# Kernel optimization log

Hardware: AMD Instinct MI355X
Metric: run time of the kernel (lower is better)

The kernel has to match this reference:

```python
import jax, jax.numpy as jnp
import numpy as np

NUM_HEADS = 2
POOL_K = 256
REPEAT = 20


def setup_inputs() -> dict:
    key = jax.random.key(0)
    k1, k2, k3 = jax.random.split(key, 3)
    C = 6144
    d = C // NUM_HEADS                      # 3072
    N = REPEAT * (d // POOL_K)              # 240, required by Pq add
    x = jax.random.normal(k1, (N, C), dtype=jnp.float32)
    w_qkv = jax.random.normal(k2, (3 * C, C), dtype=jnp.float32) * 0.02
    w_proj = jax.random.normal(k3, (C, C), dtype=jnp.float32) * 0.02
    b_proj = jnp.zeros((C,), dtype=jnp.float32)
    return {"x": x, "w_qkv": w_qkv, "w_proj": w_proj, "b_proj": b_proj}


def reference(x, w_qkv, w_proj, b_proj):
    N, C = x.shape
    H = NUM_HEADS
    d = C // H
    scale = d ** -0.5
    # qkv: (N, 3C) -> (N, 3, H, d) -> (3, H, N, d)
    qkv = (x @ w_qkv.T).reshape(N, 3, H, d).transpose(1, 2, 0, 3)
    q, k, v = qkv[0], qkv[1], qkv[2]        # each (H, N, d)
    # MaxPool1d(256) over last dim, then tile x20 along last dim -> (H, N, N)
    Pq = q.reshape(H, N, d // POOL_K, POOL_K).max(axis=-1)
    Pq = jnp.tile(Pq, (1, 1, REPEAT))       # (H, N, N)
    attn = jnp.einsum('hnd,hmd->hnm', q, k) * scale + 0.1 * Pq
    attn = jax.nn.softmax(attn, axis=-1)
    out = jnp.einsum('hnm,hmd->hnd', attn, v)    # (H, N, d)
    out = out.transpose(1, 0, 2).reshape(N, C)
    return out @ w_proj.T + b_proj
```

## Files before the change

### kernel.cpp

```cpp
#include <hip/hip_runtime.h>
#include <hip/hip_bf16.h>

#define NN 240
#define CC 6144
#define DD 3072
#define C3 18432
#define HH 2

typedef __attribute__((ext_vector_type(8))) short bf16x8;
typedef __attribute__((ext_vector_type(4))) float f32x4;
typedef unsigned short ushort_t;

static __device__ __forceinline__ unsigned short f2bf(float f) {
    __hip_bfloat16 h = __float2bfloat16(f);
    return __builtin_bit_cast(unsigned short, h);
}

#define GLDS16(g, l) __builtin_amdgcn_global_load_lds( \
    (const __attribute__((address_space(1))) void*)(g), \
    (__attribute__((address_space(3))) void*)(l), 16, 0, 0)

__global__ __launch_bounds__(512, 4)
void gemm_bt4(const ushort_t* __restrict__ Ab, int lda, long long sAz,
              const float* __restrict__ B, int ldb, long long sBz,
              const float* __restrict__ bias,
              float* __restrict__ C0, long long sC0z,
              float* __restrict__ CP, long long sCPz,
              int ldc, int N, int Kc, int KS,
              ushort_t* __restrict__ Qb) {
    __shared__ ushort_t sA[2][256 * 64];
    __shared__ ushort_t sB[2][64 * 64];

    const int zc = blockIdx.z;
    const int z = zc / KS, kc = zc % KS;
    const ushort_t* Abase = Ab + (size_t)z * sAz + (size_t)kc * Kc;
    const float*    Bbase = B  + (size_t)z * sBz + (size_t)kc * Kc;
    float* Cw = (kc == 0) ? (C0 + (size_t)z * sC0z)
                          : (CP + (size_t)(z * (KS - 1) + kc - 1) * sCPz);

    const int n0 = blockIdx.x * 64;
    const int tid = threadIdx.x, lane = tid & 63, wid = tid >> 6;
    const int wm = wid >> 1, wn = wid & 1;
    const int l16 = lane & 15, lk = lane >> 4;

    const int arow = wid * 32 + (lane >> 3);
    const ushort_t* ap = Abase + (size_t)arow * lda
                         + ((lane & 7) ^ ((lane >> 3) & 7)) * 8;

    const int brow = tid >> 3, boct = tid & 7;
    const float* bp = Bbase + (size_t)(n0 + brow) * ldb + boct * 8;
    const int bws = brow * 64 + ((boct ^ (brow & 7)) * 8);

    f32x4 acc[4][2] = {};
    const int nt = Kc / 64;

    {
#pragma unroll
        for (int i = 0; i < 4; ++i)
            GLDS16(ap + (size_t)i * 8 * lda, &sA[0][(wid * 4 + i) * 512]);
        float4 f0 = *(const float4*)bp;
        float4 f1 = *(const float4*)(bp + 4);
        asm volatile("s_waitcnt vmcnt(0)" ::: "memory");
        bf16x8 r;
        r[0] = (short)f2bf(f0.x); r[1] = (short)f2bf(f0.y);
        r[2] = (short)f2bf(f0.z); r[3] = (short)f2bf(f0.w);
        r[4] = (short)f2bf(f1.x); r[5] = (short)f2bf(f1.y);
        r[6] = (short)f2bf(f1.z); r[7] = (short)f2bf(f1.w);
        *(bf16x8*)&sB[0][bws] = r;
        __syncthreads();
    }

    for (int t = 0; t < nt; ++t) {
        const int cur = t & 1, nxt = cur ^ 1;
        const bool pf = (t + 1 < nt);
        float4 f0, f1;
        if (pf) {
            const ushort_t* a = ap + (size_t)(t + 1) * 64;
#pragma unroll
            for (int i = 0; i < 4; ++i)
                GLDS16(a + (size_t)i * 8 * lda, &sA[nxt][(wid * 4 + i) * 512]);
            const float* p = bp + (size_t)(t + 1) * 64;
            f0 = *(const float4*)p;
            f1 = *(const float4*)(p + 4);
        }
        __builtin_amdgcn_sched_barrier(0);

        const char* As = (const char*)sA[cur];
        const char* Bs = (const char*)sB[cur];
#pragma unroll
        for (int ks = 0; ks < 2; ++ks) {
            bf16x8 af[4], bf[2];
#pragma unroll
            for (int mt = 0; mt < 4; ++mt) {
                int row = wm * 64 + mt * 16 + l16;
                int boff = row * 128 + (((ks * 4 + lk) * 16) ^ ((row & 7) << 4));
                af[mt] = *(const bf16x8*)(As + boff);
            }
#pragma unroll
            for (int nf = 0; nf < 2; ++nf) {
                int row = wn * 32 + nf * 16 + l16;
                int boff = row * 128 + (((ks * 4 + lk) * 16) ^ ((row & 7) << 4));
                bf[nf] = *(const bf16x8*)(Bs + boff);
            }
            __builtin_amdgcn_s_setprio(1);
#pragma unroll
            for (int mt = 0; mt < 4; ++mt)
#pragma unroll
                for (int nf = 0; nf < 2; ++nf)
                    acc[mt][nf] = __builtin_amdgcn_mfma_f32_16x16x32_bf16(
                        af[mt], bf[nf], acc[mt][nf], 0, 0, 0);
            __builtin_amdgcn_s_setprio(0);
        }
        __builtin_amdgcn_sched_barrier(0);

        if (pf) {
            asm volatile("s_waitcnt vmcnt(0)" ::: "memory");
            bf16x8 r;
            r[0] = (short)f2bf(f0.x); r[1] = (short)f2bf(f0.y);
            r[2] = (short)f2bf(f0.z); r[3] = (short)f2bf(f0.w);
            r[4] = (short)f2bf(f1.x); r[5] = (short)f2bf(f1.y);
            r[6] = (short)f2bf(f1.z); r[7] = (short)f2bf(f1.w);
            *(bf16x8*)&sB[nxt][bws] = r;
        }
        __syncthreads();
    }

#pragma unroll
    for (int mt = 0; mt < 4; ++mt) {
#pragma unroll
        for (int j = 0; j < 4; ++j) {
            int grow = wm * 64 + mt * 16 + lk * 4 + j;
            if (grow < NN) {
#pragma unroll
                for (int nf = 0; nf < 2; ++nf) {
                    int gcol = n0 + wn * 32 + nf * 16 + l16;
                    if (gcol < N) {
                        float v = acc[mt][nf][j];
                        if (kc == 0 && bias) v += bias[gcol];
                        Cw[(size_t)grow * ldc + gcol] = v;
                        if (Qb && gcol < CC)
                            Qb[(size_t)grow * CC + gcol] = f2bf(v);
                    }
                }
            }
        }
    }
}

__global__ __launch_bounds__(256)
void convert_kernel(const float* __restrict__ x, ushort_t* __restrict__ xb) {
    int id = blockIdx.x * 256 + threadIdx.x;
    int row = id / 768, c8 = id % 768;
    bf16x8 o = {};
    if (row < NN) {
        const float* p = x + (size_t)row * CC + c8 * 8;
        float4 a = *(const float4*)p, b = *(const float4*)(p + 4);
        o[0] = (short)f2bf(a.x); o[1] = (short)f2bf(a.y);
        o[2] = (short)f2bf(a.z); o[3] = (short)f2bf(a.w);
        o[4] = (short)f2bf(b.x); o[5] = (short)f2bf(b.y);
        o[6] = (short)f2bf(b.z); o[7] = (short)f2bf(b.w);
    }
    *(bf16x8*)(xb + (size_t)row * CC + c8 * 8) = o;
}

__global__ __launch_bounds__(256)
void reduce_proj(float4* __restrict__ o4, const float4* __restrict__ p4,
                 long long s4) {
    int i = blockIdx.x * 256 + threadIdx.x;
    float4 a = o4[i];
#pragma unroll
    for (int k = 0; k < 2; ++k) {
        float4 b = p4[(size_t)k * s4 + i];
        a.x += b.x; a.y += b.y; a.z += b.z; a.w += b.w;
    }
    o4[i] = a;
}

__global__ __launch_bounds__(256)
void qmax_kernel(const float* __restrict__ qkv, float* __restrict__ qmax) {
    int idx = blockIdx.x * 4 + (threadIdx.x >> 6);
    int lane = threadIdx.x & 63;
    int c = idx % 12;
    int r = idx / 12;
    int n = r % NN, h = r / NN;
    const float* p = qkv + (size_t)n * C3 + h * DD + c * 256 + lane * 4;
    float4 f = *(const float4*)p;
    float m = fmaxf(fmaxf(f.x, f.y), fmaxf(f.z, f.w));
#pragma unroll
    for (int off = 32; off >= 1; off >>= 1)
        m = fmaxf(m, __shfl_xor(m, off));
    if (lane == 0) qmax[idx] = m;
}

__global__ __launch_bounds__(256)
void softmax_kernel(float* __restrict__ attn, const float* __restrict__ gpart,
                    int ksm1, const float* __restrict__ qmax) {
    int r = blockIdx.x * 4 + (threadIdx.x >> 6);
    int lane = threadIdx.x & 63;
    int z = r / NN, n = r % NN;
    float* row = attn + (size_t)r * NN;
    const float* qm = qmax + r * 12;
    const float scale = 0.0180421959f;
    float v[4];
    float mx = -1e30f;
#pragma unroll
    for (int i = 0; i < 4; ++i) {
        int m = lane + 64 * i;
        v[i] = -1e30f;
        if (m < NN) {
            float s = row[m];
            for (int kc = 0; kc < ksm1; ++kc)
                s += gpart[(size_t)(z * ksm1 + kc) * (NN * NN)
                           + (size_t)n * NN + m];
            v[i] = s * scale + 0.1f * qm[m % 12];
        }
        mx = fmaxf(mx, v[i]);
    }
#pragma unroll
    for (int off = 32; off >= 1; off >>= 1)
        mx = fmaxf(mx, __shfl_xor(mx, off));
    float s = 0.f;
#pragma unroll
    for (int i = 0; i < 4; ++i) {
        v[i] = __expf(v[i] - mx);
        s += v[i];
    }
#pragma unroll
    for (int off = 32; off >= 1; off >>= 1)
        s += __shfl_xor(s, off);
    float inv = 1.0f / s;
#pragma unroll
    for (int i = 0; i < 4; ++i) {
        int m = lane + 64 * i;
        if (m < NN) row[m] = v[i] * inv;
    }
}

__global__ __launch_bounds__(256)
void pv_kernel(const float* __restrict__ attn, const float* __restrict__ qkv,
               ushort_t* __restrict__ preb) {
    const int h = blockIdx.z;
    const int n0 = blockIdx.y * 16;
    const int dd0 = blockIdx.x * 256;
    __shared__ float s_attn[16 * NN];
    for (int i = threadIdx.x; i < 16 * NN; i += 256)
        s_attn[i] = attn[(size_t)h * NN * NN + (n0 + i / NN) * NN + (i % NN)];
    __syncthreads();

    const float* vp = qkv + 2 * CC + h * DD + dd0 + threadIdx.x;
    float acc[16] = {};
    for (int m = 0; m < NN; m += 4) {
        float v0 = vp[(size_t)(m + 0) * C3];
        float v1 = vp[(size_t)(m + 1) * C3];
        float v2 = vp[(size_t)(m + 2) * C3];
        float v3 = vp[(size_t)(m + 3) * C3];
#pragma unroll
        for (int i = 0; i < 16; ++i) {
            float4 a = *(const float4*)&s_attn[i * NN + m];
            acc[i] += a.x * v0 + a.y * v1 + a.z * v2 + a.w * v3;
        }
    }
#pragma unroll
    for (int i = 0; i < 16; ++i)
        preb[(size_t)(n0 + i) * CC + h * DD + dd0 + threadIdx.x] =
            f2bf(acc[i]);
}

extern "C" void kernel_launch(void* const* d_in, const int* in_sizes, int n_in,
                              void* d_out, int out_size, void* d_ws, size_t ws_size,
                              hipStream_t stream) {
    const float* x      = (const float*)d_in[0];
    const float* w_qkv  = (const float*)d_in[1];
    const float* w_proj = (const float*)d_in[2];
    const float* b_proj = (const float*)d_in[3];
    float* out = (float*)d_out;

    const size_t f_qkv  = (size_t)NN * C3;
    const size_t f_attn = (size_t)HH * NN * NN;
    const size_t f_qmax = (size_t)HH * NN * 12;
    float* qkv   = (float*)d_ws;
    float* attn  = qkv + f_qkv;
    float* qmaxb = attn + f_attn;
    ushort_t* xb   = (ushort_t*)(qmaxb + f_qmax);
    ushort_t* qb   = xb + (size_t)256 * CC;
    ushort_t* preb = qb + (size_t)256 * CC;
    float* gpart = (float*)(preb + (size_t)256 * CC);

    convert_kernel<<<768, 256, 0, stream>>>(x, xb);

    gemm_bt4<<<dim3(C3 / 64, 1, 1), 512, 0, stream>>>(
        xb, CC, 0LL, w_qkv, CC, 0LL, nullptr,
        qkv, 0LL, gpart, 0LL,
        C3, C3, CC, 1, qb);

    qmax_kernel<<<1440, 256, 0, stream>>>(qkv, qmaxb);

    gemm_bt4<<<dim3(4, 1, HH * 16), 512, 0, stream>>>(
        qb, CC, (long long)DD,
        qkv + CC, C3, (long long)DD, nullptr,
        attn, (long long)(NN * NN), gpart, (long long)(NN * NN),
        NN, NN, DD / 16, 16, nullptr);

    softmax_kernel<<<120, 256, 0, stream>>>(attn, gpart, 15, qmaxb);

    pv_kernel<<<dim3(12, 15, HH), 256, 0, stream>>>(attn, qkv, preb);

    gemm_bt4<<<dim3(CC / 64, 1, 3), 512, 0, stream>>>(
        preb, CC, 0LL, w_proj, CC, 0LL, b_proj,
        out, 0LL, gpart, (long long)((size_t)NN * CC),
        CC, CC, CC / 3, 3, nullptr);
    reduce_proj<<<1440, 256, 0, stream>>>((float4*)out, (const float4*)gpart,
        (long long)((size_t)NN * CC / 4));
}
```

Baseline: 354.2 us.

## Deepen GEMM B-operand prefetch to two stages and raise QK split-K to 24

Restructures the bf16 MFMA GEMM main loop so the fp32 B tile is loaded two iterations ahead into alternating register sets. Waits use partial vmcnt counts instead of draining all outstanding loads, and the loop is unrolled by two so the register buffers swap roles. The aim is to hide global-load latency of the fp32 weight stream, which dominates these memory-bound GEMMs. Separately, the QK^T GEMM split-K grows from 16 to 24 chunks for more parallelism, with the softmax summing 23 partials. The unroll-by-two loop assumes an even tile count, and extra registers may lower occupancy.

```diff
diff --git a/kernel.cpp b/kernel.cpp
--- a/kernel.cpp
+++ b/kernel.cpp
@@ -21,13 +21,13 @@
     (__attribute__((address_space(3))) void*)(l), 16, 0, 0)
 
 __global__ __launch_bounds__(512, 4)
-void gemm_bt4(const ushort_t* __restrict__ Ab, int lda, long long sAz,
-              const float* __restrict__ B, int ldb, long long sBz,
-              const float* __restrict__ bias,
-              float* __restrict__ C0, long long sC0z,
-              float* __restrict__ CP, long long sCPz,
-              int ldc, int N, int Kc, int KS,
-              ushort_t* __restrict__ Qb) {
+void gemm_p2(const ushort_t* __restrict__ Ab, int lda, long long sAz,
+             const float* __restrict__ B, int ldb, long long sBz,
+             const float* __restrict__ bias,
+             float* __restrict__ C0, long long sC0z,
+             float* __restrict__ CP, long long sCPz,
+             int ldc, int N, int Kc, int KS,
+             ushort_t* __restrict__ Qb) {
     __shared__ ushort_t sA[2][256 * 64];
     __shared__ ushort_t sB[2][64 * 64];
 
@@ -51,42 +51,31 @@
     const float* bp = Bbase + (size_t)(n0 + brow) * ldb + boct * 8;
     const int bws = brow * 64 + ((boct ^ (brow & 7)) * 8);
 
+    const int nt = Kc / 64;
     f32x4 acc[4][2] = {};
-    const int nt = Kc / 64;
-
-    {
+
+    auto ISSUE_A = [&](int t) {
+        const ushort_t* a = ap + (size_t)t * 64;
 #pragma unroll
         for (int i = 0; i < 4; ++i)
-            GLDS16(ap + (size_t)i * 8 * lda, &sA[0][(wid * 4 + i) * 512]);
-        float4 f0 = *(const float4*)bp;
-        float4 f1 = *(const float4*)(bp + 4);
-        asm volatile("s_waitcnt vmcnt(0)" ::: "memory");
+            GLDS16(a + (size_t)i * 8 * lda, &sA[t & 1][(wid * 4 + i) * 512]);
+    };
+    auto LOAD_B = [&](int t, float4& g0, float4& g1) {
+        const float* p = bp + (size_t)t * 64;
+        g0 = *(const float4*)p;
+        g1 = *(const float4*)(p + 4);
+    };
+    auto WRITE_B = [&](int t, float4& g0, float4& g1) {
         bf16x8 r;
-        r[0] = (short)f2bf(f0.x); r[1] = (short)f2bf(f0.y);
-        r[2] = (short)f2bf(f0.z); r[3] = (short)f2bf(f0.w);
-        r[4] = (short)f2bf(f1.x); r[5] = (short)f2bf(f1.y);
-        r[6] = (short)f2bf(f1.z); r[7] = (short)f2bf(f1.w);
-        *(bf16x8*)&sB[0][bws] = r;
-        __syncthreads();
-    }
-
-    for (int t = 0; t < nt; ++t) {
-        const int cur = t & 1, nxt = cur ^ 1;
-        const bool pf = (t + 1 < nt);
-        float4 f0, f1;
-        if (pf) {
-            const ushort_t* a = ap + (size_t)(t + 1) * 64;
-#pragma unroll
-            for (int i = 0; i < 4; ++i)
-                GLDS16(a + (size_t)i * 8 * lda, &sA[nxt][(wid * 4 + i) * 512]);
-            const float* p = bp + (size_t)(t + 1) * 64;
-            f0 = *(const float4*)p;
-            f1 = *(const float4*)(p + 4);
-        }
-        __builtin_amdgcn_sched_barrier(0);
-
-        const char* As = (const char*)sA[cur];
-        const char* Bs = (const char*)sB[cur];
+        r[0] = (short)f2bf(g0.x); r[1] = (short)f2bf(g0.y);
+        r[2] = (short)f2bf(g0.z); r[3] = (short)f2bf(g0.w);
+        r[4] = (short)f2bf(g1.x); r[5] = (short)f2bf(g1.y);
+        r[6] = (short)f2bf(g1.z); r[7] = (short)f2bf(g1.w);
+        *(bf16x8*)&sB[t & 1][bws] = r;
+    };
+    auto MFMA_PH = [&](int t) {
+        const char* As = (const char*)sA[t & 1];
+        const char* Bs = (const char*)sB[t & 1];
 #pragma unroll
         for (int ks = 0; ks < 2; ++ks) {
             bf16x8 af[4], bf[2];
@@ -111,18 +100,42 @@
                         af[mt], bf[nf], acc[mt][nf], 0, 0, 0);
             __builtin_amdgcn_s_setprio(0);
         }
+    };
+
+    float4 e0, e1, o0, o1;
+
+    ISSUE_A(0);
+    LOAD_B(0, e0, e1);
+    if (nt > 1) {
+        LOAD_B(1, o0, o1);
+        asm volatile("s_waitcnt vmcnt(2)" ::: "memory");
+    } else {
+        asm volatile("s_waitcnt vmcnt(0)" ::: "memory");
+    }
+    __builtin_amdgcn_sched_barrier(0);
+    WRITE_B(0, e0, e1);
+    asm volatile("s_waitcnt lgkmcnt(0)" ::: "memory");
+    __builtin_amdgcn_s_barrier();
+
+    auto STEP = [&](int t, float4& w0, float4& w1, float4& r0, float4& r1) {
+        const bool ia = (t + 1 < nt);
+        const bool ib = (t + 2 < nt);
+        if (ia) ISSUE_A(t + 1);
+        if (ib) LOAD_B(t + 2, w0, w1);
         __builtin_amdgcn_sched_barrier(0);
-
-        if (pf) {
-            asm volatile("s_waitcnt vmcnt(0)" ::: "memory");
-            bf16x8 r;
-            r[0] = (short)f2bf(f0.x); r[1] = (short)f2bf(f0.y);
-            r[2] = (short)f2bf(f0.z); r[3] = (short)f2bf(f0.w);
-            r[4] = (short)f2bf(f1.x); r[5] = (short)f2bf(f1.y);
-            r[6] = (short)f2bf(f1.z); r[7] = (short)f2bf(f1.w);
-            *(bf16x8*)&sB[nxt][bws] = r;
-        }
-        __syncthreads();
+        MFMA_PH(t);
+        __builtin_amdgcn_sched_barrier(0);
+        if (ib) asm volatile("s_waitcnt vmcnt(2)" ::: "memory");
+        else    asm volatile("s_waitcnt vmcnt(0)" ::: "memory");
+        __builtin_amdgcn_sched_barrier(0);
+        if (ia) WRITE_B(t + 1, r0, r1);
+        asm volatile("s_waitcnt lgkmcnt(0)" ::: "memory");
+        __builtin_amdgcn_s_barrier();
+    };
+
+    for (int t = 0; t < nt; t += 2) {
+        STEP(t,     e0, e1, o0, o1);
+        STEP(t + 1, o0, o1, e0, e1);
     }
 
 #pragma unroll
@@ -288,24 +301,24 @@
 
     convert_kernel<<<768, 256, 0, stream>>>(x, xb);
 
-    gemm_bt4<<<dim3(C3 / 64, 1, 1), 512, 0, stream>>>(
+    gemm_p2<<<dim3(C3 / 64, 1, 1), 512, 0, stream>>>(
         xb, CC, 0LL, w_qkv, CC, 0LL, nullptr,
         qkv, 0LL, gpart, 0LL,
         C3, C3, CC, 1, qb);
 
     qmax_kernel<<<1440, 256, 0, stream>>>(qkv, qmaxb);
 
-    gemm_bt4<<<dim3(4, 1, HH * 16), 512, 0, stream>>>(
+    gemm_p2<<<dim3(4, 1, HH * 24), 512, 0, stream>>>(
         qb, CC, (long long)DD,
         qkv + CC, C3, (long long)DD, nullptr,
         attn, (long long)(NN * NN), gpart, (long long)(NN * NN),
-        NN, NN, DD / 16, 16, nullptr);
-
-    softmax_kernel<<<120, 256, 0, stream>>>(attn, gpart, 15, qmaxb);
+        NN, NN, DD / 24, 24, nullptr);
+
+    softmax_kernel<<<120, 256, 0, stream>>>(attn, gpart, 23, qmaxb);
 
     pv_kernel<<<dim3(12, 15, HH), 256, 0, stream>>>(attn, qkv, preb);
 
-    gemm_bt4<<<dim3(CC / 64, 1, 3), 512, 0, stream>>>(
+    gemm_p2<<<dim3(CC / 64, 1, 3), 512, 0, stream>>>(
         preb, CC, 0LL, w_proj, CC, 0LL, b_proj,
         out, 0LL, gpart, (long long)((size_t)NN * CC),
         CC, CC, CC / 3, 3, nullptr);
```

Measured after the change: 341.6 us. 3.6% less time.
